# Kernel tuning notes

Measured on AMD Instinct MI355X. Metric: run time of the kernel, lower is better.

## Reference

```python
import jax, jax.numpy as jnp
import numpy as np

N = 100000      # nodes
E = 1600000     # directed edges (avg degree 16)
F_IN = 128      # in_channels
H = 128         # hidden
G = 64          # graphs in batch


def setup_inputs() -> dict:
    key = jax.random.key(0)
    ks = jax.random.split(key, 9)
    x = jax.random.normal(ks[0], (N, F_IN), dtype=jnp.float32)
    edge_index = jax.random.randint(ks[1], (2, E), 0, N, dtype=jnp.int32)
    batch = jnp.sort(jax.random.randint(ks[2], (N,), 0, G, dtype=jnp.int32))
    # GCNConv weights (glorot-ish scale) and biases
    W1 = jax.random.normal(ks[3], (F_IN, H), dtype=jnp.float32) / np.sqrt(F_IN)
    b1 = jnp.zeros((H,), dtype=jnp.float32)
    W2 = jax.random.normal(ks[4], (H, H // 2), dtype=jnp.float32) / np.sqrt(H)
    b2 = jnp.zeros((H // 2,), dtype=jnp.float32)
    lin_w = jax.random.normal(ks[5], (H // 2, 1), dtype=jnp.float32) / np.sqrt(H // 2)
    lin_b = jnp.zeros((1,), dtype=jnp.float32)
    return {"x": x, "edge_index": edge_index, "batch": batch,
            "W1": W1, "b1": b1, "W2": W2, "b2": b2,
            "lin_w": lin_w, "lin_b": lin_b}


def reference(x, edge_index, batch, W1, b1, W2, b2, lin_w, lin_b):
    n = x.shape[0]
    # GCN default: add self-loops, symmetric deg^-1/2 normalization
    loop = jnp.arange(n, dtype=edge_index.dtype)
    src = jnp.concatenate([edge_index[0], loop])
    dst = jnp.concatenate([edge_index[1], loop])
    deg = jax.ops.segment_sum(jnp.ones_like(dst, dtype=x.dtype), dst, num_segments=n)
    dis = jax.lax.rsqrt(jnp.maximum(deg, 1.0))  # deg >= 1 due to self-loops
    norm = dis[src] * dis[dst]                  # [E+N]

    def gcn_conv(h, W, b):
        h = h @ W                               # transform first (smaller dim on edges)
        m = h[src] * norm[:, None]              # gather + scale  [E+N, d]
        return jax.ops.segment_sum(m, dst, num_segments=n) + b  # scatter-add

    h = jax.nn.relu(gcn_conv(x, W1, b1))        # dropout = identity in eval mode
    h = jax.nn.relu(gcn_conv(h, W2, b2))

    # global_mean_pool over graph ids
    sums = jax.ops.segment_sum(h, batch, num_segments=G)            # [G, H//2]
    cnt = jax.ops.segment_sum(jnp.ones((n,), h.dtype), batch, num_segments=G)
    pooled = sums / jnp.maximum(cnt, 1.0)[:, None]

    return (pooled @ lin_w + lin_b)[:, 0]       # squeeze(-1) -> [G]
```

## Files before the change

kernel.cpp:

```cpp
#include <hip/hip_runtime.h>
#include <hip/hip_fp16.h>


#define DN 512
#define DSHIFT 9
#define SLOT 80

typedef _Float16 half8 __attribute__((ext_vector_type(8)));
typedef float f32x4 __attribute__((ext_vector_type(4)));

__global__ __launch_bounds__(1024) void k_split(const int* __restrict__ src,
                                                const int* __restrict__ dst,
                                                int* __restrict__ hcnt,
                                                int* __restrict__ binned,
                                                int E, int NBK, int PB,
                                                int CAPB) {
  __shared__ int h[256];
  int t = threadIdx.x;
  int b = blockIdx.x;
  if (t < 256) h[t] = 0;
  __syncthreads();
  int base = b * 8192;
  int pk[8], bk[8];
  bool val[8];
#pragma unroll
  for (int j = 0; j < 8; ++j) {
    int i = base + j * 1024 + t;
    val[j] = (i < E);
    if (val[j]) {
      int s = src[i], d = dst[i];
      bk[j] = d >> DSHIFT;
      pk[j] = (s << DSHIFT) | (d & (DN - 1));
      atomicAdd(&h[bk[j]], 1);
    }
  }
  __syncthreads();
  for (int k = t; k < NBK; k += 1024) hcnt[k * PB + b] = min(h[k], SLOT);
  __syncthreads();
  if (t < 256) h[t] = 0;
  __syncthreads();
#pragma unroll
  for (int j = 0; j < 8; ++j) {
    if (val[j]) {
      int slot = atomicAdd(&h[bk[j]], 1);
      if (slot < SLOT) binned[bk[j] * CAPB + b * SLOT + slot] = pk[j];
    }
  }
}

__global__ __launch_bounds__(1024) void k_bucket(const int* __restrict__ binned,
                                                 const int* __restrict__ hcnt,
                                                 int2* __restrict__ rr,
                                                 float* __restrict__ dis,
                                                 int* __restrict__ esrc,
                                                 int N, int PB, int CAPB) {
  __shared__ int hc[1024];
  __shared__ int lcnt[DN];
  __shared__ int lscan[DN];
  int k = blockIdx.x;
  int t = threadIdx.x;
  int nbase = k << DSHIFT;
  for (int b2 = t; b2 < PB; b2 += 1024) hc[b2] = hcnt[k * PB + b2];
  if (t < DN) lcnt[t] = 0;
  __syncthreads();
  for (int idx = t; idx < CAPB; idx += 1024) {
    int b2 = idx / SLOT, j = idx - b2 * SLOT;
    if (j < hc[b2])
      atomicAdd(&lcnt[binned[k * CAPB + idx] & (DN - 1)], 1);
  }
  __syncthreads();
  if (t < DN) lscan[t] = lcnt[t];
  __syncthreads();
  for (int off = 1; off < DN; off <<= 1) {
    int v = (t < DN && t >= off) ? lscan[t - off] : 0;
    __syncthreads();
    if (t < DN) lscan[t] += v;
    __syncthreads();
  }
  int bstart = k * CAPB;
  if (t < DN) {
    int g = nbase + t;
    if (g < N) {
      int inc = lscan[t];
      int c = lcnt[t];
      rr[g] = make_int2(bstart + inc - c, bstart + inc);
      dis[g] = rsqrtf((float)(c + 1));
    }
    lcnt[t] = lscan[t] - lcnt[t];
  }
  __syncthreads();
  for (int idx = t; idx < CAPB; idx += 1024) {
    int b2 = idx / SLOT, j = idx - b2 * SLOT;
    if (j < hc[b2]) {
      int p = binned[k * CAPB + idx];
      int slot = atomicAdd(&lcnt[p & (DN - 1)], 1);
      esrc[bstart + slot] = (unsigned)p >> DSHIFT;
    }
  }
}

template <int COLS, int K, typename AT>
__global__ __launch_bounds__(256) void k_gemm(const AT* __restrict__ A,
                                              const float* __restrict__ W,
                                              const float* __restrict__ dis,
                                              __half* __restrict__ out, int nrows) {
  constexpr int KP = K + 8;
  __shared__ _Float16 As[64 * KP];
  __shared__ _Float16 Wt[COLS * KP];
  int t = threadIdx.x;
  int row0 = blockIdx.x * 64;

  {
    constexpr int C4 = COLS / 4;
    for (int i = t; i < K * C4; i += 256) {
      int k = i / C4, c = (i % C4) * 4;
      float4 wv = *(const float4*)&W[(size_t)k * COLS + c];
      Wt[(c + 0) * KP + k] = (_Float16)wv.x;
      Wt[(c + 1) * KP + k] = (_Float16)wv.y;
      Wt[(c + 2) * KP + k] = (_Float16)wv.z;
      Wt[(c + 3) * KP + k] = (_Float16)wv.w;
    }
  }
  if constexpr (sizeof(AT) == 4) {
    constexpr int F4 = K / 4;
    for (int id = t; id < 64 * F4; id += 256) {
      int r = id / F4, kq = (id % F4) * 4;
      int grow = row0 + r;
      float4 av = (grow < nrows) ? *(const float4*)&A[(size_t)grow * K + kq]
                                 : make_float4(0.f, 0.f, 0.f, 0.f);
      _Float16* dst = &As[r * KP + kq];
      dst[0] = (_Float16)av.x;
      dst[1] = (_Float16)av.y;
      dst[2] = (_Float16)av.z;
      dst[3] = (_Float16)av.w;
    }
  } else {
    constexpr int H8 = K / 8;
    for (int id = t; id < 64 * H8; id += 256) {
      int r = id / H8, kq = (id % H8) * 8;
      int grow = row0 + r;
      half8 av = (grow < nrows)
                     ? *(const half8*)&A[(size_t)grow * K + kq]
                     : (half8){0, 0, 0, 0, 0, 0, 0, 0};
      *(half8*)&As[r * KP + kq] = av;
    }
  }
  __syncthreads();

  int wave = t >> 6, lane = t & 63;
  int m = lane & 15;
  int quad = lane >> 4;
  constexpr int NT = COLS / 16;

  f32x4 acc[NT];
#pragma unroll
  for (int ct = 0; ct < NT; ++ct) acc[ct] = (f32x4){0.f, 0.f, 0.f, 0.f};

  const _Float16* arow = &As[(wave * 16 + m) * KP + quad * 8];
#pragma unroll
  for (int ks = 0; ks < K; ks += 32) {
    half8 af = *(const half8*)&arow[ks];
#pragma unroll
    for (int ct = 0; ct < NT; ++ct) {
      half8 bf = *(const half8*)&Wt[(ct * 16 + m) * KP + quad * 8 + ks];
      acc[ct] = __builtin_amdgcn_mfma_f32_16x16x32_f16(af, bf, acc[ct], 0, 0, 0);
    }
  }

  __syncthreads();
  _Float16* Ds = As;
  constexpr int DP = COLS + 4;
#pragma unroll
  for (int j = 0; j < 4; ++j) {
    int rl = wave * 16 + quad * 4 + j;
    int gr = row0 + rl;
    float dn = (gr < nrows) ? dis[gr] : 0.f;
#pragma unroll
    for (int ct = 0; ct < NT; ++ct)
      Ds[rl * DP + ct * 16 + m] = (_Float16)(acc[ct][j] * dn);
  }
  __syncthreads();
  constexpr int C8 = COLS / 8;
  for (int id = t; id < 64 * C8; id += 256) {
    int r = id / C8, c8 = (id % C8) * 8;
    int gr = row0 + r;
    if (gr < nrows)
      *(half8*)&out[(size_t)gr * COLS + c8] = *(const half8*)&Ds[r * DP + c8];
  }
}

template <int COLS, bool FUSE>
__global__ __launch_bounds__(256) void k_agg(const __half* __restrict__ H,
                                             const int2* __restrict__ rr,
                                             const int* __restrict__ esrc,
                                             const float* __restrict__ dis,
                                             const float* __restrict__ bias,
                                             __half* __restrict__ out,
                                             const float* __restrict__ lin_w,
                                             float* __restrict__ dnode, int n) {
  constexpr int LPE = COLS / 8;
  constexpr int NG = 64 / LPE;
  int node = (blockIdx.x * 256 + threadIdx.x) >> 6;
  if (node >= n) return;
  int lane = threadIdx.x & 63;
  int group = lane / LPE;
  int c = (lane % LPE) * 8;

  float acc[8];
#pragma unroll
  for (int j = 0; j < 8; ++j) acc[j] = 0.f;

  int2 be = rr[node];
  int end = be.y;
  int e0 = be.x + group;
  int e1 = e0 + NG;
  int s0 = 0, s1 = 0;
  float w0 = 0.f, w1 = 0.f;
  if (e0 < end) { s0 = esrc[e0]; w0 = 1.f; }
  if (e1 < end) { s1 = esrc[e1]; w1 = 1.f; }
  while (e0 < end) {
    float4 r0 = *(const float4*)&H[(size_t)s0 * COLS + c];
    float4 r1 = *(const float4*)&H[(size_t)s1 * COLS + c];
    int e2 = e0 + 2 * NG, e3 = e1 + 2 * NG;
    int s2 = 0, s3 = 0;
    float w2 = 0.f, w3 = 0.f;
    if (e2 < end) { s2 = esrc[e2]; w2 = 1.f; }
    if (e3 < end) { s3 = esrc[e3]; w3 = 1.f; }
    {
      union { float4 f4; __half2 h2[4]; } u;
      u.f4 = r0;
#pragma unroll
      for (int j = 0; j < 4; ++j) {
        float2 f = __half22float2(u.h2[j]);
        acc[2 * j + 0] = fmaf(f.x, w0, acc[2 * j + 0]);
        acc[2 * j + 1] = fmaf(f.y, w0, acc[2 * j + 1]);
      }
      u.f4 = r1;
#pragma unroll
      for (int j = 0; j < 4; ++j) {
        float2 f = __half22float2(u.h2[j]);
        acc[2 * j + 0] = fmaf(f.x, w1, acc[2 * j + 0]);
        acc[2 * j + 1] = fmaf(f.y, w1, acc[2 * j + 1]);
      }
    }
    e0 = e2; s0 = s2; w0 = w2;
    e1 = e3; s1 = s3; w1 = w3;
  }
#pragma unroll
  for (int m = LPE; m < 64; m <<= 1) {
#pragma unroll
    for (int j = 0; j < 8; ++j) acc[j] += __shfl_xor(acc[j], m, 64);
  }
  if (group == 0) {
    float dn = dis[node];
    union { float4 f4; __half2 h2[4]; } u;
    u.f4 = *(const float4*)&H[(size_t)node * COLS + c];
    float o[8];
#pragma unroll
    for (int j = 0; j < 4; ++j) {
      float2 f = __half22float2(u.h2[j]);
      o[2 * j + 0] = fmaxf(fmaf(acc[2 * j + 0] + f.x, dn, bias[c + 2 * j + 0]), 0.f);
      o[2 * j + 1] = fmaxf(fmaf(acc[2 * j + 1] + f.y, dn, bias[c + 2 * j + 1]), 0.f);
    }
    if constexpr (FUSE) {
      float part = 0.f;
#pragma unroll
      for (int j = 0; j < 8; ++j) part = fmaf(o[j], lin_w[c + j], part);
      part += __shfl_xor(part, 1, 64);
      part += __shfl_xor(part, 2, 64);
      part += __shfl_xor(part, 4, 64);
      if (lane == 0) dnode[node] = part;
    } else {
      union { __half2 h2[4]; float4 f4; } ov;
#pragma unroll
      for (int j = 0; j < 4; ++j)
        ov.h2[j] = __floats2half2_rn(o[2 * j + 0], o[2 * j + 1]);
      *(float4*)&out[(size_t)node * COLS + c] = ov.f4;
    }
  }
}

__device__ inline int lower_bound_i(const int* a, int n, int v) {
  int lo = 0, hi = n;
  while (lo < hi) {
    int m = (lo + hi) >> 1;
    if (a[m] < v) lo = m + 1; else hi = m;
  }
  return lo;
}

__global__ __launch_bounds__(256) void k_poolfinal(const float* __restrict__ dnode,
                                                   const int* __restrict__ batch,
                                                   const float* __restrict__ lin_b,
                                                   float* __restrict__ out, int N) {
  __shared__ int bounds[2];
  __shared__ float red[4];
  int g = blockIdx.x;
  int t = threadIdx.x;
  if (t == 0) bounds[0] = lower_bound_i(batch, N, g);
  if (t == 1) bounds[1] = lower_bound_i(batch, N, g + 1);
  __syncthreads();
  int lo = bounds[0], hi = bounds[1];
  float s = 0.f;
  for (int i = lo + t; i < hi; i += 256) s += dnode[i];
#pragma unroll
  for (int m = 1; m < 64; m <<= 1) s += __shfl_xor(s, m, 64);
  if ((t & 63) == 0) red[t >> 6] = s;
  __syncthreads();
  if (t == 0) {
    float sum = red[0] + red[1] + red[2] + red[3];
    float cnt = (float)(hi - lo);
    out[g] = sum / fmaxf(cnt, 1.f) + lin_b[0];
  }
}

extern "C" void kernel_launch(void* const* d_in, const int* in_sizes, int n_in,
                              void* d_out, int out_size, void* d_ws, size_t ws_size,
                              hipStream_t stream) {
  const float* x = (const float*)d_in[0];
  const int* edge = (const int*)d_in[1];
  const int* batch = (const int*)d_in[2];
  const float* W1 = (const float*)d_in[3];
  const float* b1 = (const float*)d_in[4];
  const float* W2 = (const float*)d_in[5];
  const float* b2 = (const float*)d_in[6];
  const float* lin_w = (const float*)d_in[7];
  const float* lin_b = (const float*)d_in[8];
  float* out = (float*)d_out;

  const int N = in_sizes[2];
  const int E = in_sizes[1] / 2;
  const int G = out_size;
  const int* esrc_in = edge;
  const int* edst_in = edge + E;

  char* w = (char*)d_ws;
  size_t off = 0;
  auto take = [&](size_t bytes) {
    void* p = w + off;
    off += (bytes + 255) & ~(size_t)255;
    return p;
  };
  const int NBK = (N + DN - 1) / DN;
  const int PB = (E + 8191) / 8192;
  const int CAPB = PB * SLOT;
  int* hcnt = (int*)take((size_t)NBK * PB * 4);
  int2* rr = (int2*)take((size_t)N * 8);
  float* dis = (float*)take((size_t)N * 4);
  int* esrc = (int*)take((size_t)NBK * CAPB * 4);
  __half* XW = (__half*)take((size_t)N * 128 * 2);
  __half* H = (__half*)take((size_t)N * 128 * 2);
  float* dnode = (float*)take((size_t)N * 4);
  int* binned = (int*)XW;
  (void)ws_size;
  (void)n_in;

  k_split<<<PB, 1024, 0, stream>>>(esrc_in, edst_in, hcnt, binned, E, NBK, PB,
                                   CAPB);
  k_bucket<<<NBK, 1024, 0, stream>>>(binned, hcnt, rr, dis, esrc, N, PB, CAPB);

  int gb = (N + 63) / 64;
  int ab = (int)(((size_t)N * 64 + 255) / 256);

  k_gemm<128, 128, float><<<gb, 256, 0, stream>>>(x, W1, dis, XW, N);
  k_agg<128, false><<<ab, 256, 0, stream>>>(XW, rr, esrc, dis, b1, H,
                                            nullptr, nullptr, N);

  k_gemm<64, 128, _Float16><<<gb, 256, 0, stream>>>(
      (const _Float16*)H, W2, dis, XW, N);
  k_agg<64, true><<<ab, 256, 0, stream>>>(XW, rr, esrc, dis, b2, nullptr,
                                          lin_w, dnode, N);

  k_poolfinal<<<G, 256, 0, stream>>>(dnode, batch, lin_b, out, N);
}
```

Measured before the change: 294.2 us.

## Overlap first GEMM with edge binning and fuse mean-pool into final aggregation

The first GEMM no longer needs degree scaling, so it runs in the same grid as the edge-splitting pass, with blocks partitioned by blockIdx. The source-side normalisation moves into the first aggregation as a per-edge dis[src] weight. The global mean pool is folded into the last aggregation through per-graph atomics and a last-block-done finalisation, which removes the pool kernel and the dnode buffer. The trade-offs are an extra scattered dis load per edge in layer 1, global atomics contention, and split blocks shrunk to 256 threads.

```diff
diff --git a/kernel.cpp b/kernel.cpp
--- a/kernel.cpp
+++ b/kernel.cpp
@@ -9,42 +9,152 @@
 typedef _Float16 half8 __attribute__((ext_vector_type(8)));
 typedef float f32x4 __attribute__((ext_vector_type(4)));
 
-__global__ __launch_bounds__(1024) void k_split(const int* __restrict__ src,
-                                                const int* __restrict__ dst,
-                                                int* __restrict__ hcnt,
-                                                int* __restrict__ binned,
-                                                int E, int NBK, int PB,
-                                                int CAPB) {
+template <int COLS, int K, typename AT, bool SCALE>
+__device__ __forceinline__ void gemm_body(const AT* __restrict__ A,
+                                          const float* __restrict__ W,
+                                          const float* __restrict__ dis,
+                                          __half* __restrict__ out, int nrows,
+                                          int bid) {
+  constexpr int KP = K + 8;
+  __shared__ _Float16 As[64 * KP];
+  __shared__ _Float16 Wt[COLS * KP];
+  int t = threadIdx.x;
+  int row0 = bid * 64;
+
+  {
+    constexpr int C4 = COLS / 4;
+    for (int i = t; i < K * C4; i += 256) {
+      int k = i / C4, c = (i % C4) * 4;
+      float4 wv = *(const float4*)&W[(size_t)k * COLS + c];
+      Wt[(c + 0) * KP + k] = (_Float16)wv.x;
+      Wt[(c + 1) * KP + k] = (_Float16)wv.y;
+      Wt[(c + 2) * KP + k] = (_Float16)wv.z;
+      Wt[(c + 3) * KP + k] = (_Float16)wv.w;
+    }
+  }
+  if constexpr (sizeof(AT) == 4) {
+    constexpr int F4 = K / 4;
+    for (int id = t; id < 64 * F4; id += 256) {
+      int r = id / F4, kq = (id % F4) * 4;
+      int grow = row0 + r;
+      float4 av = (grow < nrows) ? *(const float4*)&A[(size_t)grow * K + kq]
+                                 : make_float4(0.f, 0.f, 0.f, 0.f);
+      _Float16* dst = &As[r * KP + kq];
+      dst[0] = (_Float16)av.x;
+      dst[1] = (_Float16)av.y;
+      dst[2] = (_Float16)av.z;
+      dst[3] = (_Float16)av.w;
+    }
+  } else {
+    constexpr int H8 = K / 8;
+    for (int id = t; id < 64 * H8; id += 256) {
+      int r = id / H8, kq = (id % H8) * 8;
+      int grow = row0 + r;
+      half8 av = (grow < nrows)
+                     ? *(const half8*)&A[(size_t)grow * K + kq]
+                     : (half8){0, 0, 0, 0, 0, 0, 0, 0};
+      *(half8*)&As[r * KP + kq] = av;
+    }
+  }
+  __syncthreads();
+
+  int wave = t >> 6, lane = t & 63;
+  int m = lane & 15;
+  int quad = lane >> 4;
+  constexpr int NT = COLS / 16;
+
+  f32x4 acc[NT];
+#pragma unroll
+  for (int ct = 0; ct < NT; ++ct) acc[ct] = (f32x4){0.f, 0.f, 0.f, 0.f};
+
+  const _Float16* arow = &As[(wave * 16 + m) * KP + quad * 8];
+#pragma unroll
+  for (int ks = 0; ks < K; ks += 32) {
+    half8 af = *(const half8*)&arow[ks];
+#pragma unroll
+    for (int ct = 0; ct < NT; ++ct) {
+      half8 bf = *(const half8*)&Wt[(ct * 16 + m) * KP + quad * 8 + ks];
+      acc[ct] = __builtin_amdgcn_mfma_f32_16x16x32_f16(af, bf, acc[ct], 0, 0, 0);
+    }
+  }
+
+  __syncthreads();
+  _Float16* Ds = As;
+  constexpr int DP = COLS + 4;
+#pragma unroll
+  for (int j = 0; j < 4; ++j) {
+    int rl = wave * 16 + quad * 4 + j;
+    int gr = row0 + rl;
+    float dn = 1.f;
+    if constexpr (SCALE) dn = (gr < nrows) ? dis[gr] : 0.f;
+#pragma unroll
+    for (int ct = 0; ct < NT; ++ct)
+      Ds[rl * DP + ct * 16 + m] = (_Float16)(acc[ct][j] * dn);
+  }
+  __syncthreads();
+  constexpr int C8 = COLS / 8;
+  for (int id = t; id < 64 * C8; id += 256) {
+    int r = id / C8, c8 = (id % C8) * 8;
+    int gr = row0 + r;
+    if (gr < nrows)
+      *(half8*)&out[(size_t)gr * COLS + c8] = *(const half8*)&Ds[r * DP + c8];
+  }
+}
+
+template <int COLS, int K, typename AT, bool SCALE>
+__global__ __launch_bounds__(256) void k_gemm(const AT* __restrict__ A,
+                                              const float* __restrict__ W,
+                                              const float* __restrict__ dis,
+                                              __half* __restrict__ out,
+                                              int nrows) {
+  gemm_body<COLS, K, AT, SCALE>(A, W, dis, out, nrows, blockIdx.x);
+}
+
+__device__ __forceinline__ void split_body(const int* __restrict__ src,
+                                           const int* __restrict__ dst,
+                                           int* __restrict__ hcnt,
+                                           int* __restrict__ binned, int E,
+                                           int NBK, int PB, int CAPB, int b) {
   __shared__ int h[256];
   int t = threadIdx.x;
-  int b = blockIdx.x;
-  if (t < 256) h[t] = 0;
+  h[t] = 0;
   __syncthreads();
   int base = b * 8192;
-  int pk[8], bk[8];
-  bool val[8];
-#pragma unroll
-  for (int j = 0; j < 8; ++j) {
-    int i = base + j * 1024 + t;
-    val[j] = (i < E);
-    if (val[j]) {
+#pragma unroll 8
+  for (int j = 0; j < 32; ++j) {
+    int i = base + j * 256 + t;
+    if (i < E) atomicAdd(&h[dst[i] >> DSHIFT], 1);
+  }
+  __syncthreads();
+  for (int k = t; k < NBK; k += 256) hcnt[k * PB + b] = min(h[k], SLOT);
+  __syncthreads();
+  h[t] = 0;
+  __syncthreads();
+#pragma unroll 8
+  for (int j = 0; j < 32; ++j) {
+    int i = base + j * 256 + t;
+    if (i < E) {
       int s = src[i], d = dst[i];
-      bk[j] = d >> DSHIFT;
-      pk[j] = (s << DSHIFT) | (d & (DN - 1));
-      atomicAdd(&h[bk[j]], 1);
-    }
-  }
-  __syncthreads();
-  for (int k = t; k < NBK; k += 1024) hcnt[k * PB + b] = min(h[k], SLOT);
-  __syncthreads();
-  if (t < 256) h[t] = 0;
-  __syncthreads();
-#pragma unroll
-  for (int j = 0; j < 8; ++j) {
-    if (val[j]) {
-      int slot = atomicAdd(&h[bk[j]], 1);
-      if (slot < SLOT) binned[bk[j] * CAPB + b * SLOT + slot] = pk[j];
-    }
+      int bk = d >> DSHIFT;
+      int slot = atomicAdd(&h[bk], 1);
+      if (slot < SLOT)
+        binned[bk * CAPB + b * SLOT + slot] = (s << DSHIFT) | (d & (DN - 1));
+    }
+  }
+}
+
+__global__ __launch_bounds__(256) void k_fat(
+    const float* __restrict__ x, const float* __restrict__ W1,
+    __half* __restrict__ XW, int nrows, int GB, const int* __restrict__ src,
+    const int* __restrict__ dst, int* __restrict__ hcnt,
+    int* __restrict__ binned, int E, int NBK, int PB, int CAPB,
+    int* __restrict__ gstate, int nstate) {
+  if ((int)blockIdx.x < GB) {
+    gemm_body<128, 128, float, false>(x, W1, nullptr, XW, nrows, blockIdx.x);
+  } else {
+    int b = blockIdx.x - GB;
+    if (b == 0 && (int)threadIdx.x < nstate) gstate[threadIdx.x] = 0;
+    split_body(src, dst, hcnt, binned, E, NBK, PB, CAPB, b);
   }
 }
 
@@ -99,218 +209,130 @@
   }
 }
 
-template <int COLS, int K, typename AT>
-__global__ __launch_bounds__(256) void k_gemm(const AT* __restrict__ A,
-                                              const float* __restrict__ W,
-                                              const float* __restrict__ dis,
-                                              __half* __restrict__ out, int nrows) {
-  constexpr int KP = K + 8;
-  __shared__ _Float16 As[64 * KP];
-  __shared__ _Float16 Wt[COLS * KP];
-  int t = threadIdx.x;
-  int row0 = blockIdx.x * 64;
-
-  {
-    constexpr int C4 = COLS / 4;
-    for (int i = t; i < K * C4; i += 256) {
-      int k = i / C4, c = (i % C4) * 4;
-      float4 wv = *(const float4*)&W[(size_t)k * COLS + c];
-      Wt[(c + 0) * KP + k] = (_Float16)wv.x;
-      Wt[(c + 1) * KP + k] = (_Float16)wv.y;
-      Wt[(c + 2) * KP + k] = (_Float16)wv.z;
-      Wt[(c + 3) * KP + k] = (_Float16)wv.w;
-    }
-  }
-  if constexpr (sizeof(AT) == 4) {
-    constexpr int F4 = K / 4;
-    for (int id = t; id < 64 * F4; id += 256) {
-      int r = id / F4, kq = (id % F4) * 4;
-      int grow = row0 + r;
-      float4 av = (grow < nrows) ? *(const float4*)&A[(size_t)grow * K + kq]
-                                 : make_float4(0.f, 0.f, 0.f, 0.f);
-      _Float16* dst = &As[r * KP + kq];
-      dst[0] = (_Float16)av.x;
-      dst[1] = (_Float16)av.y;
-      dst[2] = (_Float16)av.z;
-      dst[3] = (_Float16)av.w;
-    }
-  } else {
-    constexpr int H8 = K / 8;
-    for (int id = t; id < 64 * H8; id += 256) {
-      int r = id / H8, kq = (id % H8) * 8;
-      int grow = row0 + r;
-      half8 av = (grow < nrows)
-                     ? *(const half8*)&A[(size_t)grow * K + kq]
-                     : (half8){0, 0, 0, 0, 0, 0, 0, 0};
-      *(half8*)&As[r * KP + kq] = av;
-    }
-  }
-  __syncthreads();
-
-  int wave = t >> 6, lane = t & 63;
-  int m = lane & 15;
-  int quad = lane >> 4;
-  constexpr int NT = COLS / 16;
-
-  f32x4 acc[NT];
-#pragma unroll
-  for (int ct = 0; ct < NT; ++ct) acc[ct] = (f32x4){0.f, 0.f, 0.f, 0.f};
-
-  const _Float16* arow = &As[(wave * 16 + m) * KP + quad * 8];
-#pragma unroll
-  for (int ks = 0; ks < K; ks += 32) {
-    half8 af = *(const half8*)&arow[ks];
-#pragma unroll
-    for (int ct = 0; ct < NT; ++ct) {
-      half8 bf = *(const half8*)&Wt[(ct * 16 + m) * KP + quad * 8 + ks];
-      acc[ct] = __builtin_amdgcn_mfma_f32_16x16x32_f16(af, bf, acc[ct], 0, 0, 0);
-    }
-  }
-
-  __syncthreads();
-  _Float16* Ds = As;
-  constexpr int DP = COLS + 4;
-#pragma unroll
-  for (int j = 0; j < 4; ++j) {
-    int rl = wave * 16 + quad * 4 + j;
-    int gr = row0 + rl;
-    float dn = (gr < nrows) ? dis[gr] : 0.f;
-#pragma unroll
-    for (int ct = 0; ct < NT; ++ct)
-      Ds[rl * DP + ct * 16 + m] = (_Float16)(acc[ct][j] * dn);
-  }
-  __syncthreads();
-  constexpr int C8 = COLS / 8;
-  for (int id = t; id < 64 * C8; id += 256) {
-    int r = id / C8, c8 = (id % C8) * 8;
-    int gr = row0 + r;
-    if (gr < nrows)
-      *(half8*)&out[(size_t)gr * COLS + c8] = *(const half8*)&Ds[r * DP + c8];
-  }
-}
-
-template <int COLS, bool FUSE>
-__global__ __launch_bounds__(256) void k_agg(const __half* __restrict__ H,
-                                             const int2* __restrict__ rr,
-                                             const int* __restrict__ esrc,
-                                             const float* __restrict__ dis,
-                                             const float* __restrict__ bias,
-                                             __half* __restrict__ out,
-                                             const float* __restrict__ lin_w,
-                                             float* __restrict__ dnode, int n) {
+template <int COLS, bool FUSE, bool EDGEW>
+__global__ __launch_bounds__(256) void k_agg(
+    const __half* __restrict__ H, const int2* __restrict__ rr,
+    const int* __restrict__ esrc, const float* __restrict__ dis,
+    const float* __restrict__ bias, __half* __restrict__ out,
+    const float* __restrict__ lin_w, const float* __restrict__ lin_b,
+    float* __restrict__ gacc, int* __restrict__ gcnt, int* __restrict__ done,
+    const int* __restrict__ batch, float* __restrict__ outg, int n, int Gn) {
   constexpr int LPE = COLS / 8;
   constexpr int NG = 64 / LPE;
-  int node = (blockIdx.x * 256 + threadIdx.x) >> 6;
-  if (node >= n) return;
-  int lane = threadIdx.x & 63;
-  int group = lane / LPE;
-  int c = (lane % LPE) * 8;
-
-  float acc[8];
-#pragma unroll
-  for (int j = 0; j < 8; ++j) acc[j] = 0.f;
-
-  int2 be = rr[node];
-  int end = be.y;
-  int e0 = be.x + group;
-  int e1 = e0 + NG;
-  int s0 = 0, s1 = 0;
-  float w0 = 0.f, w1 = 0.f;
-  if (e0 < end) { s0 = esrc[e0]; w0 = 1.f; }
-  if (e1 < end) { s1 = esrc[e1]; w1 = 1.f; }
-  while (e0 < end) {
-    float4 r0 = *(const float4*)&H[(size_t)s0 * COLS + c];
-    float4 r1 = *(const float4*)&H[(size_t)s1 * COLS + c];
-    int e2 = e0 + 2 * NG, e3 = e1 + 2 * NG;
-    int s2 = 0, s3 = 0;
-    float w2 = 0.f, w3 = 0.f;
-    if (e2 < end) { s2 = esrc[e2]; w2 = 1.f; }
-    if (e3 < end) { s3 = esrc[e3]; w3 = 1.f; }
-    {
+  __shared__ float sp[4];
+  __shared__ int sg[4];
+  __shared__ int sflag;
+  int t = threadIdx.x;
+  int node = (blockIdx.x * 256 + t) >> 6;
+  int lane = t & 63;
+  int wave = t >> 6;
+  bool valid = node < n;
+  if (!FUSE && !valid) return;
+  if (FUSE && lane == 0) sg[wave] = -1;
+
+  if (valid) {
+    int group = lane / LPE;
+    int c = (lane % LPE) * 8;
+
+    float acc[8];
+#pragma unroll
+    for (int j = 0; j < 8; ++j) acc[j] = 0.f;
+
+    int2 be = rr[node];
+    int end = be.y;
+    int e0 = be.x + group;
+    int e1 = e0 + NG;
+    int s0 = 0, s1 = 0;
+    float w0 = 0.f, w1 = 0.f;
+    if (e0 < end) { s0 = esrc[e0]; w0 = EDGEW ? dis[s0] : 1.f; }
+    if (e1 < end) { s1 = esrc[e1]; w1 = EDGEW ? dis[s1] : 1.f; }
+    while (e0 < end) {
+      float4 r0 = *(const float4*)&H[(size_t)s0 * COLS + c];
+      float4 r1 = *(const float4*)&H[(size_t)s1 * COLS + c];
+      int e2 = e0 + 2 * NG, e3 = e1 + 2 * NG;
+      int s2 = 0, s3 = 0;
+      float w2 = 0.f, w3 = 0.f;
+      if (e2 < end) { s2 = esrc[e2]; w2 = EDGEW ? dis[s2] : 1.f; }
+      if (e3 < end) { s3 = esrc[e3]; w3 = EDGEW ? dis[s3] : 1.f; }
+      {
+        union { float4 f4; __half2 h2[4]; } u;
+        u.f4 = r0;
+#pragma unroll
+        for (int j = 0; j < 4; ++j) {
+          float2 f = __half22float2(u.h2[j]);
+          acc[2 * j + 0] = fmaf(f.x, w0, acc[2 * j + 0]);
+          acc[2 * j + 1] = fmaf(f.y, w0, acc[2 * j + 1]);
+        }
+        u.f4 = r1;
+#pragma unroll
+        for (int j = 0; j < 4; ++j) {
+          float2 f = __half22float2(u.h2[j]);
+          acc[2 * j + 0] = fmaf(f.x, w1, acc[2 * j + 0]);
+          acc[2 * j + 1] = fmaf(f.y, w1, acc[2 * j + 1]);
+        }
+      }
+      e0 = e2; s0 = s2; w0 = w2;
+      e1 = e3; s1 = s3; w1 = w3;
+    }
+#pragma unroll
+    for (int m = LPE; m < 64; m <<= 1) {
+#pragma unroll
+      for (int j = 0; j < 8; ++j) acc[j] += __shfl_xor(acc[j], m, 64);
+    }
+    if (group == 0) {
+      float dn = dis[node];
       union { float4 f4; __half2 h2[4]; } u;
-      u.f4 = r0;
+      u.f4 = *(const float4*)&H[(size_t)node * COLS + c];
+      float o[8];
 #pragma unroll
       for (int j = 0; j < 4; ++j) {
         float2 f = __half22float2(u.h2[j]);
-        acc[2 * j + 0] = fmaf(f.x, w0, acc[2 * j + 0]);
-        acc[2 * j + 1] = fmaf(f.y, w0, acc[2 * j + 1]);
+        float a0 = EDGEW ? fmaf(f.x, dn, acc[2 * j + 0]) : (acc[2 * j + 0] + f.x);
+        float a1 = EDGEW ? fmaf(f.y, dn, acc[2 * j + 1]) : (acc[2 * j + 1] + f.y);
+        o[2 * j + 0] = fmaxf(fmaf(a0, dn, bias[c + 2 * j + 0]), 0.f);
+        o[2 * j + 1] = fmaxf(fmaf(a1, dn, bias[c + 2 * j + 1]), 0.f);
       }
-      u.f4 = r1;
-#pragma unroll
-      for (int j = 0; j < 4; ++j) {
-        float2 f = __half22float2(u.h2[j]);
-        acc[2 * j + 0] = fmaf(f.x, w1, acc[2 * j + 0]);
-        acc[2 * j + 1] = fmaf(f.y, w1, acc[2 * j + 1]);
+      if constexpr (FUSE) {
+        float part = 0.f;
+#pragma unroll
+        for (int j = 0; j < 8; ++j) part = fmaf(o[j], lin_w[c + j], part);
+        part += __shfl_xor(part, 1, 64);
+        part += __shfl_xor(part, 2, 64);
+        part += __shfl_xor(part, 4, 64);
+        if (lane == 0) { sp[wave] = part; sg[wave] = batch[node]; }
+      } else {
+        union { __half2 h2[4]; float4 f4; } ov;
+#pragma unroll
+        for (int j = 0; j < 4; ++j)
+          ov.h2[j] = __floats2half2_rn(o[2 * j + 0], o[2 * j + 1]);
+        *(float4*)&out[(size_t)node * COLS + c] = ov.f4;
       }
     }
-    e0 = e2; s0 = s2; w0 = w2;
-    e1 = e3; s1 = s3; w1 = w3;
-  }
-#pragma unroll
-  for (int m = LPE; m < 64; m <<= 1) {
-#pragma unroll
-    for (int j = 0; j < 8; ++j) acc[j] += __shfl_xor(acc[j], m, 64);
-  }
-  if (group == 0) {
-    float dn = dis[node];
-    union { float4 f4; __half2 h2[4]; } u;
-    u.f4 = *(const float4*)&H[(size_t)node * COLS + c];
-    float o[8];
-#pragma unroll
-    for (int j = 0; j < 4; ++j) {
-      float2 f = __half22float2(u.h2[j]);
-      o[2 * j + 0] = fmaxf(fmaf(acc[2 * j + 0] + f.x, dn, bias[c + 2 * j + 0]), 0.f);
-      o[2 * j + 1] = fmaxf(fmaf(acc[2 * j + 1] + f.y, dn, bias[c + 2 * j + 1]), 0.f);
-    }
-    if constexpr (FUSE) {
-      float part = 0.f;
-#pragma unroll
-      for (int j = 0; j < 8; ++j) part = fmaf(o[j], lin_w[c + j], part);
-      part += __shfl_xor(part, 1, 64);
-      part += __shfl_xor(part, 2, 64);
-      part += __shfl_xor(part, 4, 64);
-      if (lane == 0) dnode[node] = part;
-    } else {
-      union { __half2 h2[4]; float4 f4; } ov;
-#pragma unroll
-      for (int j = 0; j < 4; ++j)
-        ov.h2[j] = __floats2half2_rn(o[2 * j + 0], o[2 * j + 1]);
-      *(float4*)&out[(size_t)node * COLS + c] = ov.f4;
-    }
-  }
-}
-
-__device__ inline int lower_bound_i(const int* a, int n, int v) {
-  int lo = 0, hi = n;
-  while (lo < hi) {
-    int m = (lo + hi) >> 1;
-    if (a[m] < v) lo = m + 1; else hi = m;
-  }
-  return lo;
-}
-
-__global__ __launch_bounds__(256) void k_poolfinal(const float* __restrict__ dnode,
-                                                   const int* __restrict__ batch,
-                                                   const float* __restrict__ lin_b,
-                                                   float* __restrict__ out, int N) {
-  __shared__ int bounds[2];
-  __shared__ float red[4];
-  int g = blockIdx.x;
-  int t = threadIdx.x;
-  if (t == 0) bounds[0] = lower_bound_i(batch, N, g);
-  if (t == 1) bounds[1] = lower_bound_i(batch, N, g + 1);
-  __syncthreads();
-  int lo = bounds[0], hi = bounds[1];
-  float s = 0.f;
-  for (int i = lo + t; i < hi; i += 256) s += dnode[i];
-#pragma unroll
-  for (int m = 1; m < 64; m <<= 1) s += __shfl_xor(s, m, 64);
-  if ((t & 63) == 0) red[t >> 6] = s;
-  __syncthreads();
-  if (t == 0) {
-    float sum = red[0] + red[1] + red[2] + red[3];
-    float cnt = (float)(hi - lo);
-    out[g] = sum / fmaxf(cnt, 1.f) + lin_b[0];
+  }
+
+  if constexpr (FUSE) {
+    __syncthreads();
+    if (t == 0) {
+      int cg = -1, cc = 0;
+      float cs = 0.f;
+      for (int i = 0; i < 4; ++i) {
+        int g = sg[i];
+        if (g < 0) continue;
+        if (g != cg) {
+          if (cg >= 0) { atomicAdd(&gacc[cg], cs); atomicAdd(&gcnt[cg], cc); }
+          cg = g; cs = sp[i]; cc = 1;
+        } else { cs += sp[i]; ++cc; }
+      }
+      if (cg >= 0) { atomicAdd(&gacc[cg], cs); atomicAdd(&gcnt[cg], cc); }
+      __threadfence();
+      sflag = (atomicAdd(done, 1) == (int)gridDim.x - 1) ? 1 : 0;
+    }
+    __syncthreads();
+    if (sflag && t < Gn) {
+      float s = atomicAdd(&gacc[t], 0.f);
+      int c2 = atomicAdd(&gcnt[t], 0);
+      outg[t] = s / fmaxf((float)c2, 1.f) + lin_b[0];
+    }
   }
 }
 
@@ -350,26 +372,27 @@
   int* esrc = (int*)take((size_t)NBK * CAPB * 4);
   __half* XW = (__half*)take((size_t)N * 128 * 2);
   __half* H = (__half*)take((size_t)N * 128 * 2);
-  float* dnode = (float*)take((size_t)N * 4);
-  int* binned = (int*)XW;
+  int* gstate = (int*)take((size_t)(2 * G + 1) * 4);
+  int* binned = (int*)H;
+  float* gacc = (float*)gstate;
+  int* gcnt = gstate + G;
+  int* done = gstate + 2 * G;
   (void)ws_size;
   (void)n_in;
 
-  k_split<<<PB, 1024, 0, stream>>>(esrc_in, edst_in, hcnt, binned, E, NBK, PB,
-                                   CAPB);
+  int GB = (N + 63) / 64;
+  int ab = (int)(((size_t)N * 64 + 255) / 256);
+
+  k_fat<<<GB + PB, 256, 0, stream>>>(x, W1, XW, N, GB, esrc_in, edst_in, hcnt,
+                                     binned, E, NBK, PB, CAPB, gstate,
+                                     2 * G + 1);
   k_bucket<<<NBK, 1024, 0, stream>>>(binned, hcnt, rr, dis, esrc, N, PB, CAPB);
-
-  int gb = (N + 63) / 64;
-  int ab = (int)(((size_t)N * 64 + 255) / 256);
-
-  k_gemm<128, 128, float><<<gb, 256, 0, stream>>>(x, W1, dis, XW, N);
-  k_agg<128, false><<<ab, 256, 0, stream>>>(XW, rr, esrc, dis, b1, H,
-                                            nullptr, nullptr, N);
-
-  k_gemm<64, 128, _Float16><<<gb, 256, 0, stream>>>(
+  k_agg<128, false, true><<<ab, 256, 0, stream>>>(
+      XW, rr, esrc, dis, b1, H, nullptr, nullptr, nullptr, nullptr, nullptr,
+      nullptr, nullptr, N, 0);
+  k_gemm<64, 128, _Float16, true><<<GB, 256, 0, stream>>>(
       (const _Float16*)H, W2, dis, XW, N);
-  k_agg<64, true><<<ab, 256, 0, stream>>>(XW, rr, esrc, dis, b2, nullptr,
-                                          lin_w, dnode, N);
-
-  k_poolfinal<<<G, 256, 0, stream>>>(dnode, batch, lin_b, out, N);
-}
+  k_agg<64, true, false><<<ab, 256, 0, stream>>>(
+      XW, rr, esrc, dis, b2, nullptr, lin_w, lin_b, gacc, gcnt, done, batch,
+      out, N, G);
+}
```

Result: slower. 888.7 us (+202.1%).

## Replace two-pass bucketed CSR build with fixed-capacity per-node atomic slots

Applied to the files above, without the earlier changes.

Removes the split/bucket sort kernels and instead builds the adjacency in one pass. Each edge takes a slot via a global atomicAdd on its destination's degree counter and writes its source into a fixed CAP=48 slot array per node. The degree normalisation is recomputed from the counts in the GEMM and aggregation kernels, and a small prep kernel converts and transposes the weights to fp16 once so the GEMMs can load them directly. This trades shared-memory binning and a prefix scan for contended global atomics and a padded adjacency layout. Any node with more than 48 in-edges would be silently truncated.

```diff
diff --git a/kernel.cpp b/kernel.cpp
--- a/kernel.cpp
+++ b/kernel.cpp
@@ -2,108 +2,44 @@
 #include <hip/hip_fp16.h>
 
 
-#define DN 512
-#define DSHIFT 9
-#define SLOT 80
+#define CAP 48
 
 typedef _Float16 half8 __attribute__((ext_vector_type(8)));
+typedef _Float16 half4v __attribute__((ext_vector_type(4)));
 typedef float f32x4 __attribute__((ext_vector_type(4)));
 
-__global__ __launch_bounds__(1024) void k_split(const int* __restrict__ src,
-                                                const int* __restrict__ dst,
-                                                int* __restrict__ hcnt,
-                                                int* __restrict__ binned,
-                                                int E, int NBK, int PB,
-                                                int CAPB) {
-  __shared__ int h[256];
-  int t = threadIdx.x;
-  int b = blockIdx.x;
-  if (t < 256) h[t] = 0;
-  __syncthreads();
-  int base = b * 8192;
-  int pk[8], bk[8];
-  bool val[8];
-#pragma unroll
-  for (int j = 0; j < 8; ++j) {
-    int i = base + j * 1024 + t;
-    val[j] = (i < E);
-    if (val[j]) {
-      int s = src[i], d = dst[i];
-      bk[j] = d >> DSHIFT;
-      pk[j] = (s << DSHIFT) | (d & (DN - 1));
-      atomicAdd(&h[bk[j]], 1);
-    }
-  }
-  __syncthreads();
-  for (int k = t; k < NBK; k += 1024) hcnt[k * PB + b] = min(h[k], SLOT);
-  __syncthreads();
-  if (t < 256) h[t] = 0;
-  __syncthreads();
-#pragma unroll
-  for (int j = 0; j < 8; ++j) {
-    if (val[j]) {
-      int slot = atomicAdd(&h[bk[j]], 1);
-      if (slot < SLOT) binned[bk[j] * CAPB + b * SLOT + slot] = pk[j];
-    }
-  }
-}
-
-__global__ __launch_bounds__(1024) void k_bucket(const int* __restrict__ binned,
-                                                 const int* __restrict__ hcnt,
-                                                 int2* __restrict__ rr,
-                                                 float* __restrict__ dis,
-                                                 int* __restrict__ esrc,
-                                                 int N, int PB, int CAPB) {
-  __shared__ int hc[1024];
-  __shared__ int lcnt[DN];
-  __shared__ int lscan[DN];
-  int k = blockIdx.x;
-  int t = threadIdx.x;
-  int nbase = k << DSHIFT;
-  for (int b2 = t; b2 < PB; b2 += 1024) hc[b2] = hcnt[k * PB + b2];
-  if (t < DN) lcnt[t] = 0;
-  __syncthreads();
-  for (int idx = t; idx < CAPB; idx += 1024) {
-    int b2 = idx / SLOT, j = idx - b2 * SLOT;
-    if (j < hc[b2])
-      atomicAdd(&lcnt[binned[k * CAPB + idx] & (DN - 1)], 1);
-  }
-  __syncthreads();
-  if (t < DN) lscan[t] = lcnt[t];
-  __syncthreads();
-  for (int off = 1; off < DN; off <<= 1) {
-    int v = (t < DN && t >= off) ? lscan[t - off] : 0;
-    __syncthreads();
-    if (t < DN) lscan[t] += v;
-    __syncthreads();
-  }
-  int bstart = k * CAPB;
-  if (t < DN) {
-    int g = nbase + t;
-    if (g < N) {
-      int inc = lscan[t];
-      int c = lcnt[t];
-      rr[g] = make_int2(bstart + inc - c, bstart + inc);
-      dis[g] = rsqrtf((float)(c + 1));
-    }
-    lcnt[t] = lscan[t] - lcnt[t];
-  }
-  __syncthreads();
-  for (int idx = t; idx < CAPB; idx += 1024) {
-    int b2 = idx / SLOT, j = idx - b2 * SLOT;
-    if (j < hc[b2]) {
-      int p = binned[k * CAPB + idx];
-      int slot = atomicAdd(&lcnt[p & (DN - 1)], 1);
-      esrc[bstart + slot] = (unsigned)p >> DSHIFT;
-    }
-  }
-}
-
-template <int COLS, int K, typename AT>
+__global__ __launch_bounds__(256) void k_prep(const float* __restrict__ W1,
+                                              const float* __restrict__ W2,
+                                              _Float16* __restrict__ W1t,
+                                              _Float16* __restrict__ W2t,
+                                              int* __restrict__ deg, int N) {
+  int T = gridDim.x * 256;
+  int i0 = blockIdx.x * 256 + threadIdx.x;
+  for (int i = i0; i < N; i += T) deg[i] = 0;
+  for (int i = i0; i < 128 * 128; i += T)
+    W1t[(i & 127) * 128 + (i >> 7)] = (_Float16)W1[i];
+  for (int i = i0; i < 128 * 64; i += T)
+    W2t[(i & 63) * 128 + (i >> 6)] = (_Float16)W2[i];
+}
+
+__global__ __launch_bounds__(256) void k_build(const int* __restrict__ src,
+                                               const int* __restrict__ dst,
+                                               int* __restrict__ deg,
+                                               int* __restrict__ esrc, int E) {
+  int stride = gridDim.x * 256;
+  for (int i = blockIdx.x * 256 + threadIdx.x; i < E; i += stride) {
+    int s = src[i], d = dst[i];
+    int slot = atomicAdd(&deg[d], 1);
+    if (slot < CAP) esrc[(size_t)d * CAP + slot] = s;
+  }
+}
+
+template <int COLS, int K, typename AT, bool SCALE>
 __global__ __launch_bounds__(256) void k_gemm(const AT* __restrict__ A,
-                                              const float* __restrict__ W,
-                                              const float* __restrict__ dis,
-                                              __half* __restrict__ out, int nrows) {
+                                              const _Float16* __restrict__ Wt_g,
+                                              const int* __restrict__ deg,
+                                              __half* __restrict__ out,
+                                              int nrows) {
   constexpr int KP = K + 8;
   __shared__ _Float16 As[64 * KP];
   __shared__ _Float16 Wt[COLS * KP];
@@ -111,14 +47,10 @@
   int row0 = blockIdx.x * 64;
 
   {
-    constexpr int C4 = COLS / 4;
-    for (int i = t; i < K * C4; i += 256) {
-      int k = i / C4, c = (i % C4) * 4;
-      float4 wv = *(const float4*)&W[(size_t)k * COLS + c];
-      Wt[(c + 0) * KP + k] = (_Float16)wv.x;
-      Wt[(c + 1) * KP + k] = (_Float16)wv.y;
-      Wt[(c + 2) * KP + k] = (_Float16)wv.z;
-      Wt[(c + 3) * KP + k] = (_Float16)wv.w;
+    constexpr int K8 = K / 8;
+    for (int i = t; i < COLS * K8; i += 256) {
+      int c = i / K8, k8 = (i % K8) * 8;
+      *(half8*)&Wt[c * KP + k8] = *(const half8*)&Wt_g[c * K + k8];
     }
   }
   if constexpr (sizeof(AT) == 4) {
@@ -128,11 +60,9 @@
       int grow = row0 + r;
       float4 av = (grow < nrows) ? *(const float4*)&A[(size_t)grow * K + kq]
                                  : make_float4(0.f, 0.f, 0.f, 0.f);
-      _Float16* dst = &As[r * KP + kq];
-      dst[0] = (_Float16)av.x;
-      dst[1] = (_Float16)av.y;
-      dst[2] = (_Float16)av.z;
-      dst[3] = (_Float16)av.w;
+      half4v hv = {(_Float16)av.x, (_Float16)av.y, (_Float16)av.z,
+                   (_Float16)av.w};
+      *(half4v*)&As[r * KP + kq] = hv;
     }
   } else {
     constexpr int H8 = K / 8;
@@ -174,7 +104,9 @@
   for (int j = 0; j < 4; ++j) {
     int rl = wave * 16 + quad * 4 + j;
     int gr = row0 + rl;
-    float dn = (gr < nrows) ? dis[gr] : 0.f;
+    float dn = 1.f;
+    if constexpr (SCALE)
+      dn = (gr < nrows) ? rsqrtf((float)(deg[gr] + 1)) : 0.f;
 #pragma unroll
     for (int ct = 0; ct < NT; ++ct)
       Ds[rl * DP + ct * 16 + m] = (_Float16)(acc[ct][j] * dn);
@@ -191,9 +123,8 @@
 
 template <int COLS, bool FUSE>
 __global__ __launch_bounds__(256) void k_agg(const __half* __restrict__ H,
-                                             const int2* __restrict__ rr,
                                              const int* __restrict__ esrc,
-                                             const float* __restrict__ dis,
+                                             const int* __restrict__ deg,
                                              const float* __restrict__ bias,
                                              __half* __restrict__ out,
                                              const float* __restrict__ lin_w,
@@ -210,9 +141,10 @@
 #pragma unroll
   for (int j = 0; j < 8; ++j) acc[j] = 0.f;
 
-  int2 be = rr[node];
-  int end = be.y;
-  int e0 = be.x + group;
+  int dg = deg[node];
+  int b0 = node * CAP;
+  int end = b0 + min(dg, CAP);
+  int e0 = b0 + group;
   int e1 = e0 + NG;
   int s0 = 0, s1 = 0;
   float w0 = 0.f, w1 = 0.f;
@@ -252,7 +184,7 @@
     for (int j = 0; j < 8; ++j) acc[j] += __shfl_xor(acc[j], m, 64);
   }
   if (group == 0) {
-    float dn = dis[node];
+    float dn = rsqrtf((float)(dg + 1));
     union { float4 f4; __half2 h2[4]; } u;
     u.f4 = *(const float4*)&H[(size_t)node * COLS + c];
     float o[8];
@@ -341,35 +273,27 @@
     off += (bytes + 255) & ~(size_t)255;
     return p;
   };
-  const int NBK = (N + DN - 1) / DN;
-  const int PB = (E + 8191) / 8192;
-  const int CAPB = PB * SLOT;
-  int* hcnt = (int*)take((size_t)NBK * PB * 4);
-  int2* rr = (int2*)take((size_t)N * 8);
-  float* dis = (float*)take((size_t)N * 4);
-  int* esrc = (int*)take((size_t)NBK * CAPB * 4);
+  int* deg = (int*)take((size_t)N * 4);
+  int* esrc = (int*)take((size_t)N * CAP * 4);
   __half* XW = (__half*)take((size_t)N * 128 * 2);
   __half* H = (__half*)take((size_t)N * 128 * 2);
   float* dnode = (float*)take((size_t)N * 4);
-  int* binned = (int*)XW;
+  _Float16* W1t = (_Float16*)take((size_t)128 * 128 * 2);
+  _Float16* W2t = (_Float16*)take((size_t)64 * 128 * 2);
   (void)ws_size;
   (void)n_in;
 
-  k_split<<<PB, 1024, 0, stream>>>(esrc_in, edst_in, hcnt, binned, E, NBK, PB,
-                                   CAPB);
-  k_bucket<<<NBK, 1024, 0, stream>>>(binned, hcnt, rr, dis, esrc, N, PB, CAPB);
-
-  int gb = (N + 63) / 64;
+  int GB = (N + 63) / 64;
   int ab = (int)(((size_t)N * 64 + 255) / 256);
 
-  k_gemm<128, 128, float><<<gb, 256, 0, stream>>>(x, W1, dis, XW, N);
-  k_agg<128, false><<<ab, 256, 0, stream>>>(XW, rr, esrc, dis, b1, H,
-                                            nullptr, nullptr, N);
-
-  k_gemm<64, 128, _Float16><<<gb, 256, 0, stream>>>(
-      (const _Float16*)H, W2, dis, XW, N);
-  k_agg<64, true><<<ab, 256, 0, stream>>>(XW, rr, esrc, dis, b2, nullptr,
-                                          lin_w, dnode, N);
-
+  k_prep<<<400, 256, 0, stream>>>(W1, W2, W1t, W2t, deg, N);
+  k_build<<<1024, 256, 0, stream>>>(esrc_in, edst_in, deg, esrc, E);
+  k_gemm<128, 128, float, true><<<GB, 256, 0, stream>>>(x, W1t, deg, XW, N);
+  k_agg<128, false><<<ab, 256, 0, stream>>>(XW, esrc, deg, b1, H, nullptr,
+                                            nullptr, N);
+  k_gemm<64, 128, _Float16, true><<<GB, 256, 0, stream>>>(
+      (const _Float16*)H, W2t, deg, XW, N);
+  k_agg<64, true><<<ab, 256, 0, stream>>>(XW, esrc, deg, b2, nullptr, lin_w,
+                                          dnode, N);
   k_poolfinal<<<G, 256, 0, stream>>>(dnode, batch, lin_b, out, N);
 }
```

Measured after the change: 375.4 us. 27.6% more time.
